# Kernel tuning notes

Hardware: AMD Instinct MI355X
Metric: run time of the kernel (lower is better)

Reference implementation:

```python
import jax, jax.numpy as jnp
import numpy as np

DIM = 4096
N_HEADS = 32
N_KV = 8
HEAD_DIM = 128
BATCH = 32
CACHE_LEN = 2048 + 128  # hard-coded in init_kv_cache
START_POS = 2047
ROPE_BASE = 10000.0


def setup_inputs() -> dict:
    key = jax.random.key(0)
    ks = jax.random.split(key, 5)
    qkv_dim = (N_HEADS + 2 * N_KV) * HEAD_DIM  # fused QKV width
    return {
        "x": jax.random.normal(ks[0], (BATCH, DIM), jnp.float32) * 0.02,
        "wqkv": jax.random.normal(ks[1], (DIM, qkv_dim), jnp.float32) * 0.02,
        "wo": jax.random.normal(ks[2], (DIM, DIM), jnp.float32) * 0.02,
        "cache_k": jax.random.normal(ks[3], (BATCH, N_KV, CACHE_LEN, HEAD_DIM), jnp.float32) * 0.02,
        "cache_v": jax.random.normal(ks[4], (BATCH, N_KV, CACHE_LEN, HEAD_DIM), jnp.float32) * 0.02,
        "start_pos": START_POS,
    }


def _rope_cos_sin(pos):
    # Llama half-split RoPE; equivalent to the head_dim x head_dim rotation matrix
    half = HEAD_DIM // 2
    inv_freq = 1.0 / (ROPE_BASE ** (jnp.arange(half, dtype=jnp.float32) * 2.0 / HEAD_DIM))
    ang = pos * inv_freq
    cos = jnp.concatenate([jnp.cos(ang), jnp.cos(ang)])
    sin = jnp.concatenate([jnp.sin(ang), jnp.sin(ang)])
    return cos, sin


def _rotate_half(t):
    h = t.shape[-1] // 2
    return jnp.concatenate([-t[..., h:], t[..., :h]], axis=-1)


def reference(x, wqkv, wo, cache_k, cache_v, start_pos):
    scale = 1.0 / np.sqrt(HEAD_DIM)
    n_rep = N_HEADS // N_KV

    # fused QKV projection
    qkv = x @ wqkv  # (B, (H + 2*K) * D)
    q = qkv[:, : N_HEADS * HEAD_DIM].reshape(BATCH, N_KV, n_rep, HEAD_DIM)
    k = qkv[:, N_HEADS * HEAD_DIM : (N_HEADS + N_KV) * HEAD_DIM].reshape(BATCH, N_KV, HEAD_DIM)
    v = qkv[:, (N_HEADS + N_KV) * HEAD_DIM :].reshape(BATCH, N_KV, HEAD_DIM)

    # RoPE at position start_pos (rotation-matrix form in the original)
    cos, sin = _rope_cos_sin(jnp.float32(start_pos))
    q = q * cos + _rotate_half(q) * sin
    k = k * cos + _rotate_half(k) * sin

    # KV cache update at start_pos
    cache_k = cache_k.at[:, :, start_pos, :].set(k)
    cache_v = cache_v.at[:, :, start_pos, :].set(v)

    # grouped-query attention over the whole (masked) cache
    scores = jnp.einsum("bgrd,bgsd->bgrs", q, cache_k) * scale  # (B, KV, rep, S)
    valid = jnp.arange(CACHE_LEN) <= start_pos
    scores = jnp.where(valid[None, None, None, :], scores, jnp.float32(-1e9))
    probs = jax.nn.softmax(scores, axis=-1)
    attn = jnp.einsum("bgrs,bgsd->bgrd", probs, cache_v).reshape(BATCH, DIM)

    # output projection
    return attn @ wo
```

## Files before the change

### kernel.cpp

```cpp
#include <hip/hip_runtime.h>
#include <math.h>

#define DIM 4096
#define NH 32
#define NKV 8
#define HD 128
#define BATCH 32
#define CL 2176
#define QKV_DIM 6144
#define NREP 4

template<int N>
__global__ void gemm_partial(const float* __restrict__ x, const float* __restrict__ w,
                             float* __restrict__ part) {
    __shared__ float xs[128 * 36];
    const int t = threadIdx.x;
    const int n0 = blockIdx.x * 256;
    const int k0 = blockIdx.y * 128;

    for (int i = 0; i < 16; ++i) {
        int e = t + i * 256;
        int b = e >> 7;
        int kk = e & 127;
        xs[kk * 36 + b] = x[(size_t)b * DIM + k0 + kk];
    }
    __syncthreads();

    float acc[32];
#pragma unroll
    for (int b = 0; b < 32; ++b) acc[b] = 0.f;

    const float* wp = w + (size_t)k0 * N + n0 + t;
    for (int kk = 0; kk < 128; ++kk) {
        float wv = wp[(size_t)kk * N];
        const float4* xr = (const float4*)&xs[kk * 36];
#pragma unroll
        for (int b4 = 0; b4 < 8; ++b4) {
            float4 xv = xr[b4];
            acc[b4 * 4 + 0] += xv.x * wv;
            acc[b4 * 4 + 1] += xv.y * wv;
            acc[b4 * 4 + 2] += xv.z * wv;
            acc[b4 * 4 + 3] += xv.w * wv;
        }
    }

    float* pp = part + (size_t)blockIdx.y * 32 * N + n0 + t;
#pragma unroll
    for (int b = 0; b < 32; ++b) pp[(size_t)b * N] = acc[b];
}

__global__ void qkv_finish(const float* __restrict__ part, const int* __restrict__ sp_p,
                           float* __restrict__ fin) {
    const int b = blockIdx.x, h = blockIdx.y, d = threadIdx.x;
    const int sp = *sp_p;
    const int col = h * 128 + d;

    float s = 0.f;
    for (int kc = 0; kc < 32; ++kc)
        s += part[(size_t)kc * 32 * QKV_DIM + (size_t)b * QKV_DIM + col];

    __shared__ float v[128];
    float outv = s;
    if (h < 40) {
        v[d] = s;
        __syncthreads();
        int j = d & 63;
        float inv_freq = powf(10000.0f, -(float)(2 * j) / 128.0f);
        float ang = (float)sp * inv_freq;
        float c = cosf(ang), sn = sinf(ang);
        float rot = (d < 64) ? -v[d + 64] : v[d - 64];
        outv = s * c + rot * sn;
    }
    fin[((size_t)b * 48 + h) * 128 + d] = outv;
}

__global__ void attn_scores(const float* __restrict__ fin, const float* __restrict__ cache_k,
                            const int* __restrict__ sp_p, float* __restrict__ scores) {
    const int bg = blockIdx.x;
    const int b = bg >> 3, g = bg & 7;
    const int sp = *sp_p;
    const int t = threadIdx.x;
    const int w = t >> 6, lane = t & 63, sl = lane & 31, half = lane >> 5;

    float4 qf[4];
#pragma unroll
    for (int h = 0; h < 4; ++h)
        qf[h] = *(const float4*)(fin + ((size_t)b * 48 + g * 4 + h) * 128 + sl * 4);

    const float scale = 0.08838834764831845f;
    const float* kbase = cache_k + ((size_t)b * NKV + g) * CL * HD;
    const float* knew = fin + ((size_t)b * 48 + 32 + g) * 128;

    const int s_begin = blockIdx.y * 1088;
    const int s_end = s_begin + 1088;

    for (int i = s_begin + w * 2; i < s_end; i += 32) {
        int s = i + half;
        const float* krow = (s == sp) ? knew : (kbase + (size_t)s * HD);
        float4 kv = *(const float4*)(krow + sl * 4);

        float p[4];
#pragma unroll
        for (int h = 0; h < 4; ++h)
            p[h] = qf[h].x * kv.x + qf[h].y * kv.y + qf[h].z * kv.z + qf[h].w * kv.w;

#pragma unroll
        for (int off = 1; off < 32; off <<= 1) {
#pragma unroll
            for (int h = 0; h < 4; ++h) p[h] += __shfl_xor(p[h], off);
        }

        if (sl == 0) {
            bool valid = (s <= sp);
            float4 sc;
            sc.x = valid ? p[0] * scale : -1e9f;
            sc.y = valid ? p[1] * scale : -1e9f;
            sc.z = valid ? p[2] * scale : -1e9f;
            sc.w = valid ? p[3] * scale : -1e9f;
            *(float4*)(scores + ((size_t)bg * CL + s) * 4) = sc;
        }
    }
}

__global__ void softmax_k(float* __restrict__ scores) {
    const int bg = blockIdx.x, h = blockIdx.y, t = threadIdx.x;
    float* sb = scores + (size_t)bg * CL * 4 + h;

    float vals[9];
    float m = -1e30f;
#pragma unroll
    for (int i = 0; i < 9; ++i) {
        int s = t + i * 256;
        vals[i] = (s < CL) ? sb[(size_t)s * 4] : -1e30f;
        m = fmaxf(m, vals[i]);
    }
#pragma unroll
    for (int off = 1; off < 64; off <<= 1) m = fmaxf(m, __shfl_xor(m, off));
    __shared__ float redm[4];
    const int w = t >> 6, lane = t & 63;
    if (lane == 0) redm[w] = m;
    __syncthreads();
    m = fmaxf(fmaxf(redm[0], redm[1]), fmaxf(redm[2], redm[3]));

    float l = 0.f;
#pragma unroll
    for (int i = 0; i < 9; ++i) {
        float e = expf(vals[i] - m);
        vals[i] = e;
        l += e;
    }
#pragma unroll
    for (int off = 1; off < 64; off <<= 1) l += __shfl_xor(l, off);
    __shared__ float redl[4];
    if (lane == 0) redl[w] = l;
    __syncthreads();
    l = redl[0] + redl[1] + redl[2] + redl[3];

    float inv = 1.f / l;
#pragma unroll
    for (int i = 0; i < 9; ++i) {
        int s = t + i * 256;
        if (s < CL) sb[(size_t)s * 4] = vals[i] * inv;
    }
}

__global__ void attn_pv(const float* __restrict__ scores, const float* __restrict__ cache_v,
                        const float* __restrict__ fin, const int* __restrict__ sp_p,
                        float* __restrict__ attn) {
    const int bg = blockIdx.x;
    const int b = bg >> 3, g = bg & 7;
    const int sp = *sp_p;
    const int t = threadIdx.x;
    const int grp = t >> 5, sl = t & 31;

    const float* vbase = cache_v + ((size_t)b * NKV + g) * CL * HD;
    const float* vnew = fin + ((size_t)b * 48 + 40 + g) * 128;
    const float* pb = scores + (size_t)bg * CL * 4;

    float o[4][4];
#pragma unroll
    for (int h = 0; h < 4; ++h)
#pragma unroll
        for (int c = 0; c < 4; ++c) o[h][c] = 0.f;

    for (int s = grp; s < CL; s += 32) {
        const float* vrow = (s == sp) ? vnew : (vbase + (size_t)s * HD);
        float4 vv = *(const float4*)(vrow + sl * 4);
        float4 pp = *(const float4*)(pb + (size_t)s * 4);
        o[0][0] += pp.x * vv.x; o[0][1] += pp.x * vv.y; o[0][2] += pp.x * vv.z; o[0][3] += pp.x * vv.w;
        o[1][0] += pp.y * vv.x; o[1][1] += pp.y * vv.y; o[1][2] += pp.y * vv.z; o[1][3] += pp.y * vv.w;
        o[2][0] += pp.z * vv.x; o[2][1] += pp.z * vv.y; o[2][2] += pp.z * vv.z; o[2][3] += pp.z * vv.w;
        o[3][0] += pp.w * vv.x; o[3][1] += pp.w * vv.y; o[3][2] += pp.w * vv.z; o[3][3] += pp.w * vv.w;
    }

    __shared__ float red[32 * 512];
#pragma unroll
    for (int h = 0; h < 4; ++h)
        *(float4*)&red[grp * 512 + h * 128 + sl * 4] = make_float4(o[h][0], o[h][1], o[h][2], o[h][3]);
    __syncthreads();

    for (int step = 16; step >= 1; step >>= 1) {
        if (grp < step) {
#pragma unroll
            for (int i = 0; i < 16; ++i) {
                int j = sl + i * 32;
                red[grp * 512 + j] += red[(grp + step) * 512 + j];
            }
        }
        __syncthreads();
    }

    if (t < 512) {
        int h = t >> 7, d = t & 127;
        attn[(size_t)b * DIM + (g * 4 + h) * 128 + d] = red[h * 128 + d];
    }
}

__global__ void out_reduce(const float* __restrict__ part, float* __restrict__ out) {
    const int e = blockIdx.x * 256 + threadIdx.x;
    float s = 0.f;
    for (int kc = 0; kc < 32; ++kc) s += part[(size_t)kc * 32 * DIM + e];
    out[e] = s;
}

extern "C" void kernel_launch(void* const* d_in, const int* in_sizes, int n_in,
                              void* d_out, int out_size, void* d_ws, size_t ws_size,
                              hipStream_t stream) {
    const float* x       = (const float*)d_in[0];
    const float* wqkv    = (const float*)d_in[1];
    const float* wo      = (const float*)d_in[2];
    const float* cache_k = (const float*)d_in[3];
    const float* cache_v = (const float*)d_in[4];
    const int*   sp      = (const int*)d_in[5];
    float* out = (float*)d_out;
    float* ws  = (float*)d_ws;

    float* part1  = ws;
    float* fin    = part1 + 6291456;
    float* scores = fin + 196608;
    float* attn   = scores + 2228224;
    float* part2  = attn + 131072;

    gemm_partial<QKV_DIM><<<dim3(24, 32), 256, 0, stream>>>(x, wqkv, part1);
    qkv_finish<<<dim3(32, 48), 128, 0, stream>>>(part1, sp, fin);
    attn_scores<<<dim3(256, 2), 1024, 0, stream>>>(fin, cache_k, sp, scores);
    softmax_k<<<dim3(256, 4), 256, 0, stream>>>(scores);
    attn_pv<<<256, 1024, 0, stream>>>(scores, cache_v, fin, sp, attn);
    gemm_partial<DIM><<<dim3(16, 32), 256, 0, stream>>>(attn, wo, part2);
    out_reduce<<<512, 256, 0, stream>>>(part2, out);
}
```

Baseline: 737.5 us.

## Fuse softmax into PV kernel, skip masked positions, read x directly in GEMM

Softmax is merged into the PV kernel: probabilities are kept in shared memory and normalization is deferred to the final output, which removes a kernel launch and a global round trip of the scores. The score and PV loops skip cache positions past start_pos, avoiding K/V reads for masked entries. The GEMM drops its shared-memory staging of x and reads float4 rows straight from global memory with a k-unroll of 4. The PV reduction now uses a cross-half shuffle followed by a 16-wave shared-memory tree, and launch bounds are added to the kernels.

```diff
diff --git a/kernel.cpp b/kernel.cpp
--- a/kernel.cpp
+++ b/kernel.cpp
@@ -11,36 +11,32 @@
 #define NREP 4
 
 template<int N>
-__global__ void gemm_partial(const float* __restrict__ x, const float* __restrict__ w,
-                             float* __restrict__ part) {
-    __shared__ float xs[128 * 36];
+__global__ __launch_bounds__(256) void gemm_partial(const float* __restrict__ x,
+                                                    const float* __restrict__ w,
+                                                    float* __restrict__ part) {
     const int t = threadIdx.x;
     const int n0 = blockIdx.x * 256;
     const int k0 = blockIdx.y * 128;
 
-    for (int i = 0; i < 16; ++i) {
-        int e = t + i * 256;
-        int b = e >> 7;
-        int kk = e & 127;
-        xs[kk * 36 + b] = x[(size_t)b * DIM + k0 + kk];
-    }
-    __syncthreads();
-
     float acc[32];
 #pragma unroll
     for (int b = 0; b < 32; ++b) acc[b] = 0.f;
 
     const float* wp = w + (size_t)k0 * N + n0 + t;
-    for (int kk = 0; kk < 128; ++kk) {
-        float wv = wp[(size_t)kk * N];
-        const float4* xr = (const float4*)&xs[kk * 36];
-#pragma unroll
-        for (int b4 = 0; b4 < 8; ++b4) {
-            float4 xv = xr[b4];
-            acc[b4 * 4 + 0] += xv.x * wv;
-            acc[b4 * 4 + 1] += xv.y * wv;
-            acc[b4 * 4 + 2] += xv.z * wv;
-            acc[b4 * 4 + 3] += xv.w * wv;
+    const float* xp = x + k0;
+
+    for (int kk = 0; kk < 128; kk += 4) {
+        const float wv0 = wp[(size_t)(kk + 0) * N];
+        const float wv1 = wp[(size_t)(kk + 1) * N];
+        const float wv2 = wp[(size_t)(kk + 2) * N];
+        const float wv3 = wp[(size_t)(kk + 3) * N];
+#pragma unroll
+        for (int b = 0; b < 32; ++b) {
+            const float4 xv = *(const float4*)(xp + (size_t)b * DIM + kk);
+            acc[b] = fmaf(xv.x, wv0, acc[b]);
+            acc[b] = fmaf(xv.y, wv1, acc[b]);
+            acc[b] = fmaf(xv.z, wv2, acc[b]);
+            acc[b] = fmaf(xv.w, wv3, acc[b]);
         }
     }
 
@@ -74,8 +70,10 @@
     fin[((size_t)b * 48 + h) * 128 + d] = outv;
 }
 
-__global__ void attn_scores(const float* __restrict__ fin, const float* __restrict__ cache_k,
-                            const int* __restrict__ sp_p, float* __restrict__ scores) {
+__global__ __launch_bounds__(1024) void attn_scores(const float* __restrict__ fin,
+                                                    const float* __restrict__ cache_k,
+                                                    const int* __restrict__ sp_p,
+                                                    float* __restrict__ scores) {
     const int bg = blockIdx.x;
     const int b = bg >> 3, g = bg & 7;
     const int sp = *sp_p;
@@ -96,6 +94,12 @@
 
     for (int i = s_begin + w * 2; i < s_end; i += 32) {
         int s = i + half;
+        if (i > sp) {
+            if (sl == 0)
+                *(float4*)(scores + ((size_t)bg * CL + s) * 4) =
+                    make_float4(-1e9f, -1e9f, -1e9f, -1e9f);
+            continue;
+        }
         const float* krow = (s == sp) ? knew : (kbase + (size_t)s * HD);
         float4 kv = *(const float4*)(krow + sl * 4);
 
@@ -122,60 +126,92 @@
     }
 }
 
-__global__ void softmax_k(float* __restrict__ scores) {
-    const int bg = blockIdx.x, h = blockIdx.y, t = threadIdx.x;
-    float* sb = scores + (size_t)bg * CL * 4 + h;
-
-    float vals[9];
-    float m = -1e30f;
-#pragma unroll
-    for (int i = 0; i < 9; ++i) {
-        int s = t + i * 256;
-        vals[i] = (s < CL) ? sb[(size_t)s * 4] : -1e30f;
-        m = fmaxf(m, vals[i]);
-    }
-#pragma unroll
-    for (int off = 1; off < 64; off <<= 1) m = fmaxf(m, __shfl_xor(m, off));
-    __shared__ float redm[4];
-    const int w = t >> 6, lane = t & 63;
-    if (lane == 0) redm[w] = m;
-    __syncthreads();
-    m = fmaxf(fmaxf(redm[0], redm[1]), fmaxf(redm[2], redm[3]));
-
-    float l = 0.f;
-#pragma unroll
-    for (int i = 0; i < 9; ++i) {
-        float e = expf(vals[i] - m);
-        vals[i] = e;
-        l += e;
-    }
-#pragma unroll
-    for (int off = 1; off < 64; off <<= 1) l += __shfl_xor(l, off);
-    __shared__ float redl[4];
-    if (lane == 0) redl[w] = l;
-    __syncthreads();
-    l = redl[0] + redl[1] + redl[2] + redl[3];
-
-    float inv = 1.f / l;
-#pragma unroll
-    for (int i = 0; i < 9; ++i) {
-        int s = t + i * 256;
-        if (s < CL) sb[(size_t)s * 4] = vals[i] * inv;
-    }
-}
-
-__global__ void attn_pv(const float* __restrict__ scores, const float* __restrict__ cache_v,
-                        const float* __restrict__ fin, const int* __restrict__ sp_p,
-                        float* __restrict__ attn) {
+__global__ __launch_bounds__(1024) void attn_sm_pv(const float* __restrict__ scores,
+                                                   const float* __restrict__ cache_v,
+                                                   const float* __restrict__ fin,
+                                                   const int* __restrict__ sp_p,
+                                                   float* __restrict__ attn) {
     const int bg = blockIdx.x;
     const int b = bg >> 3, g = bg & 7;
     const int sp = *sp_p;
     const int t = threadIdx.x;
-    const int grp = t >> 5, sl = t & 31;
+    const int w = t >> 6, lane = t & 63;
+    const int grp = t >> 5, sl = t & 31, half = (t >> 5) & 1;
+
+    __shared__ float smem[CL * 4];
+    __shared__ float redw[16 * 4];
+    __shared__ float redl[16 * 4];
+    __shared__ float s_inv[4];
+
+    const float* sb = scores + (size_t)bg * CL * 4;
+    float4 vals[3];
+    float m[4] = {-1e30f, -1e30f, -1e30f, -1e30f};
+#pragma unroll
+    for (int i = 0; i < 3; ++i) {
+        int s = t + i * 1024;
+        vals[i] = (s < CL) ? *(const float4*)(sb + (size_t)s * 4)
+                           : make_float4(-1e30f, -1e30f, -1e30f, -1e30f);
+        m[0] = fmaxf(m[0], vals[i].x);
+        m[1] = fmaxf(m[1], vals[i].y);
+        m[2] = fmaxf(m[2], vals[i].z);
+        m[3] = fmaxf(m[3], vals[i].w);
+    }
+#pragma unroll
+    for (int off = 1; off < 64; off <<= 1) {
+#pragma unroll
+        for (int h = 0; h < 4; ++h) m[h] = fmaxf(m[h], __shfl_xor(m[h], off));
+    }
+    if (lane == 0) {
+#pragma unroll
+        for (int h = 0; h < 4; ++h) redw[w * 4 + h] = m[h];
+    }
+    __syncthreads();
+#pragma unroll
+    for (int h = 0; h < 4; ++h) {
+        float mm = redw[h];
+        for (int ww = 1; ww < 16; ++ww) mm = fmaxf(mm, redw[ww * 4 + h]);
+        m[h] = mm;
+    }
+
+    float l[4] = {0.f, 0.f, 0.f, 0.f};
+#pragma unroll
+    for (int i = 0; i < 3; ++i) {
+        int s = t + i * 1024;
+        if (s < CL) {
+            float4 e;
+            e.x = expf(vals[i].x - m[0]);
+            e.y = expf(vals[i].y - m[1]);
+            e.z = expf(vals[i].z - m[2]);
+            e.w = expf(vals[i].w - m[3]);
+            *(float4*)&smem[(size_t)s * 4] = e;
+            l[0] += e.x; l[1] += e.y; l[2] += e.z; l[3] += e.w;
+        }
+    }
+#pragma unroll
+    for (int off = 1; off < 64; off <<= 1) {
+#pragma unroll
+        for (int h = 0; h < 4; ++h) l[h] += __shfl_xor(l[h], off);
+    }
+    if (lane == 0) {
+#pragma unroll
+        for (int h = 0; h < 4; ++h) redl[w * 4 + h] = l[h];
+    }
+    __syncthreads();
+#pragma unroll
+    for (int h = 0; h < 4; ++h) {
+        float ll = redl[h];
+        for (int ww = 1; ww < 16; ++ww) ll += redl[ww * 4 + h];
+        l[h] = ll;
+    }
+    if (t == 0) {
+        s_inv[0] = 1.f / l[0];
+        s_inv[1] = 1.f / l[1];
+        s_inv[2] = 1.f / l[2];
+        s_inv[3] = 1.f / l[3];
+    }
 
     const float* vbase = cache_v + ((size_t)b * NKV + g) * CL * HD;
     const float* vnew = fin + ((size_t)b * 48 + 40 + g) * 128;
-    const float* pb = scores + (size_t)bg * CL * 4;
 
     float o[4][4];
 #pragma unroll
@@ -183,28 +219,37 @@
 #pragma unroll
         for (int c = 0; c < 4; ++c) o[h][c] = 0.f;
 
-    for (int s = grp; s < CL; s += 32) {
+    for (int s = grp; s <= sp; s += 32) {
         const float* vrow = (s == sp) ? vnew : (vbase + (size_t)s * HD);
         float4 vv = *(const float4*)(vrow + sl * 4);
-        float4 pp = *(const float4*)(pb + (size_t)s * 4);
+        float4 pp = *(const float4*)&smem[(size_t)s * 4];
         o[0][0] += pp.x * vv.x; o[0][1] += pp.x * vv.y; o[0][2] += pp.x * vv.z; o[0][3] += pp.x * vv.w;
         o[1][0] += pp.y * vv.x; o[1][1] += pp.y * vv.y; o[1][2] += pp.y * vv.z; o[1][3] += pp.y * vv.w;
         o[2][0] += pp.z * vv.x; o[2][1] += pp.z * vv.y; o[2][2] += pp.z * vv.z; o[2][3] += pp.z * vv.w;
         o[3][0] += pp.w * vv.x; o[3][1] += pp.w * vv.y; o[3][2] += pp.w * vv.z; o[3][3] += pp.w * vv.w;
     }
 
-    __shared__ float red[32 * 512];
 #pragma unroll
     for (int h = 0; h < 4; ++h)
-        *(float4*)&red[grp * 512 + h * 128 + sl * 4] = make_float4(o[h][0], o[h][1], o[h][2], o[h][3]);
-    __syncthreads();
-
-    for (int step = 16; step >= 1; step >>= 1) {
-        if (grp < step) {
-#pragma unroll
-            for (int i = 0; i < 16; ++i) {
-                int j = sl + i * 32;
-                red[grp * 512 + j] += red[(grp + step) * 512 + j];
+#pragma unroll
+        for (int c = 0; c < 4; ++c) o[h][c] += __shfl_xor(o[h][c], 32);
+
+    __syncthreads();
+
+    if (half == 0) {
+#pragma unroll
+        for (int h = 0; h < 4; ++h)
+            *(float4*)&smem[w * 512 + h * 128 + sl * 4] =
+                make_float4(o[h][0], o[h][1], o[h][2], o[h][3]);
+    }
+    __syncthreads();
+
+    for (int step = 8; step >= 1; step >>= 1) {
+        if (w < step) {
+#pragma unroll
+            for (int i = 0; i < 8; ++i) {
+                int j = lane + i * 64;
+                smem[w * 512 + j] += smem[(w + step) * 512 + j];
             }
         }
         __syncthreads();
@@ -212,7 +257,7 @@
 
     if (t < 512) {
         int h = t >> 7, d = t & 127;
-        attn[(size_t)b * DIM + (g * 4 + h) * 128 + d] = red[h * 128 + d];
+        attn[(size_t)b * DIM + (g * 4 + h) * 128 + d] = smem[h * 128 + d] * s_inv[h];
     }
 }
 
@@ -244,8 +289,7 @@
     gemm_partial<QKV_DIM><<<dim3(24, 32), 256, 0, stream>>>(x, wqkv, part1);
     qkv_finish<<<dim3(32, 48), 128, 0, stream>>>(part1, sp, fin);
     attn_scores<<<dim3(256, 2), 1024, 0, stream>>>(fin, cache_k, sp, scores);
-    softmax_k<<<dim3(256, 4), 256, 0, stream>>>(scores);
-    attn_pv<<<256, 1024, 0, stream>>>(scores, cache_v, fin, sp, attn);
+    attn_sm_pv<<<256, 1024, 0, stream>>>(scores, cache_v, fin, sp, attn);
     gemm_partial<DIM><<<dim3(16, 32), 256, 0, stream>>>(attn, wo, part2);
     out_reduce<<<512, 256, 0, stream>>>(part2, out);
 }
```

New measurement: 741.3 us. Within noise of the previous version (+0.5%).
